# Optimization experiments

Measured on AMD Instinct MI355X. Metric: run time of the kernel, lower is better.

Reference implementation:

```python
import jax, jax.numpy as jnp
import numpy as np

ROT = 0.7071  # matches the literal used in DiagPool's affine theta
EPS = 1e-5    # GroupNorm default eps


def conv2d(x, w, pad):
    # x: (N,C,H,W), w: (O,I,kh,kw)
    return jax.lax.conv_general_dilated(
        x, w, window_strides=(1, 1), padding=[(pad, pad), (pad, pad)],
        dimension_numbers=("NCHW", "OIHW", "NCHW"))


def diag_pool(x):
    """Replicates F.affine_grid + F.grid_sample (align_corners=False, bilinear,
    zeros padding) with a 45-degree rotation, then mean over H (keepdim)."""
    N, C, H, W = x.shape
    dt = x.dtype
    xn = ((2.0 * jnp.arange(W, dtype=dt) + 1.0) / W - 1.0)  # normalized x coords
    yn = ((2.0 * jnp.arange(H, dtype=dt) + 1.0) / H - 1.0)  # normalized y coords
    Yn, Xn = jnp.meshgrid(yn, xn, indexing="ij")            # (H,W)
    xs = ROT * Xn - ROT * Yn   # theta row 0
    ys = ROT * Xn + ROT * Yn   # theta row 1
    # unnormalize (align_corners=False)
    xp = ((xs + 1.0) * W - 1.0) * 0.5
    yp = ((ys + 1.0) * H - 1.0) * 0.5
    x0 = jnp.floor(xp); y0 = jnp.floor(yp)
    x1 = x0 + 1.0;      y1 = y0 + 1.0
    wx1 = xp - x0; wx0 = 1.0 - wx1
    wy1 = yp - y0; wy0 = 1.0 - wy1

    def gather(yi, xi):
        valid = ((yi >= 0) & (yi < H) & (xi >= 0) & (xi < W)).astype(dt)
        yc = jnp.clip(yi, 0, H - 1).astype(jnp.int32)
        xc = jnp.clip(xi, 0, W - 1).astype(jnp.int32)
        return x[:, :, yc, xc] * valid  # (N,C,H,W)

    rot = (gather(y0, x0) * (wy0 * wx0) + gather(y0, x1) * (wy0 * wx1)
           + gather(y1, x0) * (wy1 * wx0) + gather(y1, x1) * (wy1 * wx1))
    return rot.mean(axis=2, keepdims=True)  # (N,C,1,W)


def group_norm_per_channel(x, g, b):
    # GroupNorm(cg, cg): each channel normalized over its own (H,W)
    mu = x.mean(axis=(2, 3), keepdims=True)
    var = x.var(axis=(2, 3), keepdims=True)
    xh = (x - mu) * jax.lax.rsqrt(var + EPS)
    return xh * g[None, :, None, None] + b[None, :, None, None]


def cross_axis_encode(gx, axis_fuse_w, gn_w, gn_b):
    N, cg, H, W = gx.shape
    x_h = gx.mean(axis=3, keepdims=True)                 # (N,cg,H,1)
    x_w = gx.mean(axis=2, keepdims=True)                 # (N,cg,1,W)
    x_d = diag_pool(gx)                                  # (N,cg,1,W)
    fused = jnp.concatenate(
        [x_h, x_w.transpose(0, 1, 3, 2), x_d.transpose(0, 1, 3, 2)], axis=2)  # (N,cg,H+2W,1)
    fused = conv2d(fused, axis_fuse_w, 0)
    x_h2 = fused[:, :, :H]          # (N,cg,H,1)
    x_w2 = fused[:, :, H:H + W]     # (N,cg,W,1)
    out = gx * jax.nn.sigmoid(x_h2) * jax.nn.sigmoid(x_w2.transpose(0, 1, 3, 2))
    return group_norm_per_channel(out, gn_w, gn_b)


def setup_inputs() -> dict:
    key = jax.random.key(0)
    B, C, H, W = 8, 256, 128, 128
    G = 32
    cg = C // G  # 8
    ks = jax.random.split(key, 10)
    s = 0.1
    return {
        "x": jax.random.normal(ks[0], (B, C, H, W), jnp.float32),
        "axis_fuse_w": jax.random.normal(ks[1], (cg, cg, 1, 1), jnp.float32) * s,
        "gn_w": jnp.ones((cg,), jnp.float32),
        "gn_b": jnp.zeros((cg,), jnp.float32),
        "conv1x1_w": jax.random.normal(ks[2], (cg, cg, 1, 1), jnp.float32) * s,
        "conv3x3_w": jax.random.normal(ks[3], (cg, cg, 3, 3), jnp.float32) * s,
        "conv5x5_w": jax.random.normal(ks[4], (cg, cg, 5, 5), jnp.float32) * s,
        "scale_w": jnp.ones((3,), jnp.float32),
        "ch_gate_w": jax.random.normal(ks[5], (cg, cg, 1, 1), jnp.float32) * s,
        "sp_gate_w": jax.random.normal(ks[6], (1, cg, 1, 1), jnp.float32) * s,
        "groups": 32,
    }


def reference(x, axis_fuse_w, gn_w, gn_b, conv1x1_w, conv3x3_w, conv5x5_w,
              scale_w, ch_gate_w, sp_gate_w, groups):
    B, C, H, W = x.shape
    cg = C // groups
    N = B * groups
    gx = x.reshape(N, cg, H, W)

    xa = cross_axis_encode(gx, axis_fuse_w, gn_w, gn_b)
    xa = conv2d(xa, conv1x1_w, 0)
    xb = conv2d(gx, conv3x3_w, 1)
    xc = conv2d(gx, conv5x5_w, 2)

    sw = jax.nn.softmax(scale_w)
    x1 = sw[0] * xa + sw[1] * xb + sw[2] * xc
    x2 = xb

    def ch_gate(t):
        return jax.nn.sigmoid(conv2d(t.mean(axis=(2, 3), keepdims=True), ch_gate_w, 0))

    def sp_gate(t):
        return jax.nn.sigmoid(conv2d(t, sp_gate_w, 0))

    x1 = x1 * ch_gate(x1) * sp_gate(x1)
    x2 = x2 * ch_gate(x2) * sp_gate(x2)

    x11 = jax.nn.softmax(x1.mean(axis=(2, 3)).reshape(N, 1, cg), axis=-1)  # (N,1,cg)
    x12 = x2.reshape(N, cg, H * W)
    x21 = jax.nn.softmax(x2.mean(axis=(2, 3)).reshape(N, 1, cg), axis=-1)
    x22 = x1.reshape(N, cg, H * W)
    weights = (x11 @ x12 + x21 @ x22).reshape(N, 1, H, W)
    return (gx * jax.nn.sigmoid(weights)).reshape(B, C, H, W)
```

## Files before the change

### kernel.cpp

```cpp
#include <hip/hip_runtime.h>
#include <math.h>

#define HH 128
#define WW 128
#define CG 8
#define NN 256
#define HWSZ (HH*WW)

typedef __bf16 bf16x8 __attribute__((ext_vector_type(8)));
typedef short short8v __attribute__((ext_vector_type(8)));
typedef float f32x4 __attribute__((ext_vector_type(4)));

__device__ __forceinline__ float sigmoidf_(float x){ return 1.0f/(1.0f+__expf(-x)); }

__device__ __forceinline__ unsigned short f2bf(float x){
  union { float f; unsigned u; } v; v.f = x;
  unsigned r = v.u + 0x7fffu + ((v.u >> 16) & 1u);
  return (unsigned short)(r >> 16);
}
__device__ __forceinline__ float bf2f(unsigned short h){
  union { unsigned u; float f; } v; v.u = ((unsigned)h) << 16; return v.f;
}

__global__ void kW(const float* __restrict__ w5, const float* __restrict__ scw,
                   float* __restrict__ w5s){
  int i = blockIdx.x*256 + threadIdx.x;
  if (i >= CG*CG*25) return;
  float a = scw[0], b = scw[1], c = scw[2];
  float m = fmaxf(a, fmaxf(b, c));
  float e0 = __expf(a-m), e1 = __expf(b-m), e2 = __expf(c-m);
  float sw2 = e2 / (e0+e1+e2);
  w5s[i] = sw2 * w5[i];
}

__global__ __launch_bounds__(256) void kA1(const float* __restrict__ gx,
                                           float* __restrict__ xh_ws,
                                           float* __restrict__ xw_ws){
  int b = blockIdx.x; int n = b >> 3; int c = b & 7;
  int tid = threadIdx.x;
  __shared__ float colpart[2][WW];
  const float* img = gx + (size_t)(n*CG+c)*HWSZ;
  int w = tid & 127, half = tid >> 7;
  float acc = 0.f;
  const float* p = img + half*64*WW + w;
  for (int h = 0; h < 64; ++h) acc += p[h*WW];
  colpart[half][w] = acc;
  int h2 = tid >> 1, wh = tid & 1;
  float racc = 0.f;
  const float* rp = img + h2*WW + wh*64;
  for (int j = 0; j < 64; ++j) racc += rp[j];
  racc += __shfl_xor(racc, 1);
  __syncthreads();
  if (tid < WW) xw_ws[(n*CG+c)*WW + tid] = (colpart[0][tid] + colpart[1][tid]) * (1.0f/HH);
  if (wh == 0) xh_ws[(n*CG+c)*HH + h2] = racc * (1.0f/WW);
}

__global__ __launch_bounds__(256) void kA2(const float* __restrict__ xh_ws,
                                           const float* __restrict__ xw_ws,
                                           const float* __restrict__ afw,
                                           float* __restrict__ sig_h,
                                           float* __restrict__ sig_w){
  int n = blockIdx.x;
  int tid = threadIdx.x;
  if (tid < HH){
    int h = tid;
    float v[CG];
    #pragma unroll
    for (int c = 0; c < CG; ++c) v[c] = xh_ws[(n*CG+c)*HH + h];
    #pragma unroll
    for (int o = 0; o < CG; ++o){
      float s = 0.f;
      #pragma unroll
      for (int i = 0; i < CG; ++i) s = fmaf(afw[o*CG+i], v[i], s);
      sig_h[(n*CG+o)*HH + h] = sigmoidf_(s);
    }
  } else {
    int w = tid - 128;
    float v[CG];
    #pragma unroll
    for (int c = 0; c < CG; ++c) v[c] = xw_ws[(n*CG+c)*WW + w];
    #pragma unroll
    for (int o = 0; o < CG; ++o){
      float s = 0.f;
      #pragma unroll
      for (int i = 0; i < CG; ++i) s = fmaf(afw[o*CG+i], v[i], s);
      sig_w[(n*CG+o)*WW + w] = sigmoidf_(s);
    }
  }
}

__global__ __launch_bounds__(256) void kB(const float* __restrict__ gx,
                                          const float* __restrict__ sig_h,
                                          const float* __restrict__ sig_w,
                                          const float* __restrict__ gn_w,
                                          const float* __restrict__ gn_b,
                                          float* __restrict__ Agn,
                                          float* __restrict__ Bgn){
  int b = blockIdx.x; int n = b >> 3; int c = b & 7;
  int tid = threadIdx.x;
  __shared__ float sh[HH];
  __shared__ float swv[WW];
  __shared__ float red[16];
  if (tid < HH) sh[tid] = sig_h[(n*CG+c)*HH + tid];
  else          swv[tid-128] = sig_w[(n*CG+c)*WW + tid - 128];
  __syncthreads();
  const float* img = gx + (size_t)(n*CG+c)*HWSZ;
  float s1 = 0.f, s2 = 0.f;
  for (int idx = tid; idx < HWSZ; idx += 256){
    int h = idx >> 7, w = idx & 127;
    float t = img[idx] * sh[h] * swv[w];
    s1 += t; s2 = fmaf(t, t, s2);
  }
  #pragma unroll
  for (int off = 32; off; off >>= 1){ s1 += __shfl_down(s1, off); s2 += __shfl_down(s2, off); }
  int wv = tid >> 6, ln = tid & 63;
  if (ln == 0){ red[wv] = s1; red[8+wv] = s2; }
  __syncthreads();
  if (tid == 0){
    float S1 = red[0]+red[1]+red[2]+red[3];
    float S2 = red[8]+red[9]+red[10]+red[11];
    float mu  = S1 * (1.0f/HWSZ);
    float var = S2 * (1.0f/HWSZ) - mu*mu;
    float rstd = rsqrtf(var + 1e-5f);
    float A = rstd * gn_w[c];
    Agn[n*CG+c] = A;
    Bgn[n*CG+c] = gn_b[c] - mu*A;
  }
}

__global__ __launch_bounds__(256) void kC(const float* __restrict__ gx,
                                          const float* __restrict__ w1,
                                          const float* __restrict__ w3,
                                          const float* __restrict__ w5s,
                                          const float* __restrict__ scale_w,
                                          const float* __restrict__ spw,
                                          const float* __restrict__ sig_h,
                                          const float* __restrict__ sig_w,
                                          const float* __restrict__ Agn,
                                          const float* __restrict__ Bgn,
                                          unsigned short* __restrict__ x1m,
                                          unsigned short* __restrict__ x2m,
                                          float* __restrict__ gacc){
  __shared__ __align__(16) unsigned short tile[68*36*8];
  __shared__ __align__(16) unsigned short Bm[7][16][32];
  __shared__ __align__(16) unsigned short BmLo[7][8][32];
  __shared__ float sighs[CG][32];
  __shared__ float sigws[CG][32];
  __shared__ float constA[CG];
  __shared__ float wred[4][32];

  int tid = threadIdx.x;
  int bb = blockIdx.x;
  int n  = bb >> 4;
  int t_ = bb & 15;
  int y0 = (t_ >> 2) * 32;
  int x0 = (t_ & 3) * 32;

  float sw0, sw1;
  {
    float a = scale_w[0], b = scale_w[1], c = scale_w[2];
    float m = fmaxf(a, fmaxf(b, c));
    float e0 = __expf(a-m), e1 = __expf(b-m), e2 = __expf(c-m);
    float inv = 1.0f/(e0+e1+e2);
    sw0 = e0*inv; sw1 = e1*inv;
  }
  {
    int ic = tid >> 5, k = tid & 31;
    sighs[ic][k] = sig_h[(n*CG+ic)*HH + y0 + k];
    sigws[ic][k] = sig_w[(n*CG+ic)*WW + x0 + k];
  }
  if (tid < CG){
    float s = 0.f;
    #pragma unroll
    for (int i = 0; i < CG; ++i) s = fmaf(w1[tid*CG+i], Bgn[n*CG+i], s);
    constA[tid] = sw0 * s;
  }

  const float* base_n = gx + (size_t)n*CG*HWSZ;
  #pragma unroll
  for (int p = 0; p < 4; ++p){
    const float* i0 = base_n + (size_t)(2*p)*HWSZ;
    const float* i1 = base_n + (size_t)(2*p+1)*HWSZ;
    for (int e = tid; e < 1296; e += 256){
      int yy = e / 36, xx = e - yy*36;
      int gy = y0 + yy - 2, gz = x0 + xx - 2;
      float v0 = 0.f, v1 = 0.f;
      if ((unsigned)gy < HH && (unsigned)gz < WW){
        int o = gy*WW + gz; v0 = i0[o]; v1 = i1[o];
      }
      unsigned pk = (unsigned)f2bf(v0) | ((unsigned)f2bf(v1) << 16);
      *reinterpret_cast<unsigned*>(&tile[(yy*36 + xx)*8 + 2*p]) = pk;
    }
  }

  for (int e = tid; e < 3584; e += 256){
    int s   = e >> 9;
    int rem = e & 511;
    int nn = rem >> 5, kk = rem & 31;
    int tap = s*4 + (kk >> 3);
    int ic  = kk & 7;
    float wv = 0.f;
    if (nn < 8){
      if (tap < 25)       wv = w5s[nn*200 + ic*25 + tap];
      else if (tap == 25) wv = sw0 * w1[nn*CG + ic] * Agn[n*CG + ic];
    } else if (tap < 25){
      int ky = tap/5, kx = tap - ky*5;
      if (ky >= 1 && ky <= 3 && kx >= 1 && kx <= 3)
        wv = w3[(nn-8)*72 + ic*9 + (ky-1)*3 + (kx-1)];
    }
    unsigned short hi = f2bf(wv);
    Bm[s][nn][kk] = hi;
    if (nn < 8) BmLo[s][nn][kk] = f2bf(wv - bf2f(hi));
  }
  __syncthreads();

  #pragma unroll
  for (int p = 0; p < 4; ++p){
    for (int e = tid; e < 1024; e += 256){
      int yl = e >> 5, xl = e & 31;
      unsigned pk = *reinterpret_cast<const unsigned*>(&tile[((yl+2)*36 + xl+2)*8 + 2*p]);
      float v0 = bf2f((unsigned short)(pk & 0xffffu)) * sighs[2*p][yl]   * sigws[2*p][xl];
      float v1 = bf2f((unsigned short)(pk >> 16))     * sighs[2*p+1][yl] * sigws[2*p+1][xl];
      unsigned opk = (unsigned)f2bf(v0) | ((unsigned)f2bf(v1) << 16);
      *reinterpret_cast<unsigned*>(&tile[((yl+36)*36 + xl+2)*8 + 2*p]) = opk;
    }
  }

  int lane = tid & 63;
  int wid  = tid >> 6;
  int pr = lane & 15;
  int tg = lane >> 4;
  short8v zs = {0,0,0,0,0,0,0,0};
  bf16x8 zb = __builtin_bit_cast(bf16x8, zs);
  bf16x8 bH[7], bL[7];
  int ofs[7];
  #pragma unroll
  for (int s = 0; s < 7; ++s){
    bH[s] = *reinterpret_cast<const bf16x8*>(&Bm[s][pr][tg*8]);
    bL[s] = (pr < 8) ? *reinterpret_cast<const bf16x8*>(&BmLo[s][pr][tg*8]) : zb;
    int t = s*4 + tg;
    int ky, kx;
    if (t < 25){ ky = t/5; kx = t - ky*5; }
    else if (t == 25){ ky = 36; kx = 2; }
    else { ky = 0; kx = 0; }
    ofs[s] = (ky*36 + kx)*8;
  }
  __syncthreads();

  float cA  = (pr < 8) ? constA[pr] : 0.f;
  float spv = spw[pr & 7];
  float sAcc = 0.f, qAcc = 0.f;

  #pragma unroll 2
  for (int i = 0; i < 16; ++i){
    int mb = wid*16 + i;
    int yl = mb >> 1;
    int xh = (mb & 1) << 4;
    const unsigned short* abase = &tile[(yl*36 + xh + pr)*8];
    f32x4 accP = {0.f,0.f,0.f,0.f};
    f32x4 accQ = {0.f,0.f,0.f,0.f};
    #pragma unroll
    for (int s = 0; s < 7; ++s){
      bf16x8 a = *reinterpret_cast<const bf16x8*>(abase + ofs[s]);
      accP = __builtin_amdgcn_mfma_f32_16x16x32_bf16(a, bH[s], accP, 0, 0, 0);
      accQ = __builtin_amdgcn_mfma_f32_16x16x32_bf16(a, bL[s], accQ, 0, 0, 0);
    }
    float av[4], ot[4], vv[4], sg[4];
    #pragma unroll
    for (int r = 0; r < 4; ++r) av[r] = accP[r] + accQ[r];
    #pragma unroll
    for (int r = 0; r < 4; ++r) ot[r] = __shfl_xor(av[r], 8);
    #pragma unroll
    for (int r = 0; r < 4; ++r)
      vv[r] = (pr < 8) ? (av[r] + cA + sw1*ot[r]) : av[r];
    #pragma unroll
    for (int r = 0; r < 4; ++r){
      float t = spv * vv[r];
      t += __shfl_xor(t, 1);
      t += __shfl_xor(t, 2);
      t += __shfl_xor(t, 4);
      sg[r] = sigmoidf_(t);
    }
    ushort4 u;
    #pragma unroll
    for (int r = 0; r < 4; ++r){
      sAcc += vv[r];
      qAcc = fmaf(vv[r], sg[r], qAcc);
      ((unsigned short*)&u)[r] = f2bf(vv[r]);
    }
    int gy  = y0 + yl;
    int gxx = x0 + xh + tg*4;
    size_t off = ((size_t)(n*CG + (pr & 7))*HH + gy)*WW + gxx;
    if (pr < 8) *reinterpret_cast<ushort4*>(x1m + off) = u;
    else        *reinterpret_cast<ushort4*>(x2m + off) = u;
  }

  sAcc += __shfl_xor(sAcc, 16); sAcc += __shfl_xor(sAcc, 32);
  qAcc += __shfl_xor(qAcc, 16); qAcc += __shfl_xor(qAcc, 32);
  if (lane < 16){
    int b0 = (pr < 8) ? pr : (8 + pr);
    wred[wid][b0]     = sAcc;
    wred[wid][b0 + 8] = qAcc;
  }
  __syncthreads();
  if (tid < 32){
    float s = wred[0][tid] + wred[1][tid] + wred[2][tid] + wred[3][tid];
    atomicAdd(&gacc[n*32 + tid], s);
  }
}

__global__ void kT(const float* __restrict__ gacc, const float* __restrict__ cgw,
                   float* __restrict__ a1a2){
  int n = blockIdx.x*blockDim.x + threadIdx.x;
  if (n >= NN) return;
  const float* g = gacc + n*32;
  float m1[CG], q1[CG], m2[CG], q2[CG];
  #pragma unroll
  for (int c = 0; c < CG; ++c){
    m1[c] = g[c]      * (1.0f/HWSZ);
    q1[c] = g[8+c]    * (1.0f/HWSZ);
    m2[c] = g[16+c]   * (1.0f/HWSZ);
    q2[c] = g[24+c]   * (1.0f/HWSZ);
  }
  float chg1[CG], chg2[CG];
  #pragma unroll
  for (int o = 0; o < CG; ++o){
    float s1 = 0.f, s2 = 0.f;
    #pragma unroll
    for (int i = 0; i < CG; ++i){ s1 = fmaf(cgw[o*CG+i], m1[i], s1); s2 = fmaf(cgw[o*CG+i], m2[i], s2); }
    chg1[o] = sigmoidf_(s1); chg2[o] = sigmoidf_(s2);
  }
  float z1[CG], z2[CG];
  float mx1 = -1e30f, mx2 = -1e30f;
  #pragma unroll
  for (int c = 0; c < CG; ++c){
    z1[c] = chg1[c]*q1[c]; z2[c] = chg2[c]*q2[c];
    mx1 = fmaxf(mx1, z1[c]); mx2 = fmaxf(mx2, z2[c]);
  }
  float su1 = 0.f, su2 = 0.f;
  #pragma unroll
  for (int c = 0; c < CG; ++c){
    z1[c] = __expf(z1[c]-mx1); su1 += z1[c];
    z2[c] = __expf(z2[c]-mx2); su2 += z2[c];
  }
  float i1 = 1.0f/su1, i2 = 1.0f/su2;
  #pragma unroll
  for (int c = 0; c < CG; ++c){
    float x11 = z1[c]*i1;
    float x21 = z2[c]*i2;
    a1a2[n*16 + c]     = x21 * chg1[c];
    a1a2[n*16 + 8 + c] = x11 * chg2[c];
  }
}

__global__ __launch_bounds__(256) void kF(const float* __restrict__ gx,
                                          const unsigned short* __restrict__ x1m,
                                          const unsigned short* __restrict__ x2m,
                                          const float* __restrict__ a1a2,
                                          const float* __restrict__ spw,
                                          float* __restrict__ out){
  int tid = threadIdx.x;
  int bb = blockIdx.x;
  int n  = bb >> 6;
  int hw = ((bb & 63) << 8) + tid;
  size_t base = (size_t)(n*CG)*HWSZ + hw;
  float a1[CG], a2[CG], sp[CG];
  #pragma unroll
  for (int c = 0; c < CG; ++c){
    a1[c] = a1a2[n*16 + c];
    a2[c] = a1a2[n*16 + 8 + c];
    sp[c] = spw[c];
  }
  float d1 = 0.f, dd1 = 0.f, d2 = 0.f, dd2 = 0.f;
  #pragma unroll
  for (int c = 0; c < CG; ++c){
    float v1 = bf2f(x1m[base + (size_t)c*HWSZ]);
    float v2 = bf2f(x2m[base + (size_t)c*HWSZ]);
    d1  = fmaf(sp[c], v1, d1);  dd1 = fmaf(a1[c], v1, dd1);
    d2  = fmaf(sp[c], v2, d2);  dd2 = fmaf(a2[c], v2, dd2);
  }
  float Wv = sigmoidf_(d1)*dd1 + sigmoidf_(d2)*dd2;
  float sW = sigmoidf_(Wv);
  #pragma unroll
  for (int c = 0; c < CG; ++c)
    out[base + (size_t)c*HWSZ] = gx[base + (size_t)c*HWSZ] * sW;
}

extern "C" void kernel_launch(void* const* d_in, const int* in_sizes, int n_in,
                              void* d_out, int out_size, void* d_ws, size_t ws_size,
                              hipStream_t stream){
  const float* x   = (const float*)d_in[0];
  const float* afw = (const float*)d_in[1];
  const float* gnw = (const float*)d_in[2];
  const float* gnb = (const float*)d_in[3];
  const float* w1  = (const float*)d_in[4];
  const float* w3  = (const float*)d_in[5];
  const float* w5  = (const float*)d_in[6];
  const float* scw = (const float*)d_in[7];
  const float* cgw = (const float*)d_in[8];
  const float* spw = (const float*)d_in[9];

  char* ws = (char*)d_ws;
  float* sig_h = (float*)(ws + 0);
  float* sig_w = (float*)(ws + 1048576);
  float* Agn   = (float*)(ws + 2097152);
  float* Bgn   = (float*)(ws + 2105344);
  float* gacc  = (float*)(ws + 2113536);
  float* a1a2  = (float*)(ws + 2146304);
  float* w5s   = (float*)(ws + 2146304);
  unsigned short* x1m = (unsigned short*)(ws + 2162688);
  unsigned short* x2m = (unsigned short*)(ws + 2162688 + 67108864);
  float* out = (float*)d_out;
  float* xh_ws = (float*)d_out;
  float* xw_ws = (float*)d_out + 262144;

  hipMemsetAsync(gacc, 0, NN*32*sizeof(float), stream);
  kW <<<7, 256, 0, stream>>>(w5, scw, w5s);
  kA1<<<NN*CG, 256, 0, stream>>>(x, xh_ws, xw_ws);
  kA2<<<NN, 256, 0, stream>>>(xh_ws, xw_ws, afw, sig_h, sig_w);
  kB <<<NN*CG, 256, 0, stream>>>(x, sig_h, sig_w, gnw, gnb, Agn, Bgn);
  kC <<<NN*16, 256, 0, stream>>>(x, w1, w3, w5s, scw, spw, sig_h, sig_w, Agn, Bgn, x1m, x2m, gacc);
  kT <<<4, 64, 0, stream>>>(gacc, cgw, a1a2);
  kF <<<NN*64, 256, 0, stream>>>(x, x1m, x2m, a1a2, spw, out);
}
```

Baseline: 506.8 us.

## Fold scale mixing and spatial-gate dot into MFMA weights; vectorize tile and final kernel

```diff
diff --git a/kernel.cpp b/kernel.cpp
--- a/kernel.cpp
+++ b/kernel.cpp
@@ -14,9 +14,8 @@
 __device__ __forceinline__ float sigmoidf_(float x){ return 1.0f/(1.0f+__expf(-x)); }
 
 __device__ __forceinline__ unsigned short f2bf(float x){
-  union { float f; unsigned u; } v; v.f = x;
-  unsigned r = v.u + 0x7fffu + ((v.u >> 16) & 1u);
-  return (unsigned short)(r >> 16);
+  __bf16 h = (__bf16)x;
+  return __builtin_bit_cast(unsigned short, h);
 }
 __device__ __forceinline__ float bf2f(unsigned short h){
   union { unsigned u; float f; } v; v.u = ((unsigned)h) << 16; return v.f;
@@ -143,7 +142,7 @@
                                           float* __restrict__ gacc){
   __shared__ __align__(16) unsigned short tile[68*36*8];
   __shared__ __align__(16) unsigned short Bm[7][16][32];
-  __shared__ __align__(16) unsigned short BmLo[7][8][32];
+  __shared__ __align__(16) unsigned short BmLo[7][10][32];
   __shared__ float sighs[CG][32];
   __shared__ float sigws[CG][32];
   __shared__ float constA[CG];
@@ -177,20 +176,23 @@
   }
 
   const float* base_n = gx + (size_t)n*CG*HWSZ;
-  #pragma unroll
-  for (int p = 0; p < 4; ++p){
-    const float* i0 = base_n + (size_t)(2*p)*HWSZ;
-    const float* i1 = base_n + (size_t)(2*p+1)*HWSZ;
-    for (int e = tid; e < 1296; e += 256){
-      int yy = e / 36, xx = e - yy*36;
-      int gy = y0 + yy - 2, gz = x0 + xx - 2;
-      float v0 = 0.f, v1 = 0.f;
-      if ((unsigned)gy < HH && (unsigned)gz < WW){
-        int o = gy*WW + gz; v0 = i0[o]; v1 = i1[o];
+  for (int e = tid; e < 1296; e += 256){
+    int yy = e / 36, xx = e - yy*36;
+    int gy = y0 + yy - 2, gz = x0 + xx - 2;
+    uint4 pk;
+    unsigned* pw = (unsigned*)&pk;
+    if ((unsigned)gy < HH && (unsigned)gz < WW){
+      int o = gy*WW + gz;
+      #pragma unroll
+      for (int p = 0; p < 4; ++p){
+        float v0 = base_n[(size_t)(2*p)*HWSZ + o];
+        float v1 = base_n[(size_t)(2*p+1)*HWSZ + o];
+        pw[p] = (unsigned)f2bf(v0) | ((unsigned)f2bf(v1) << 16);
       }
-      unsigned pk = (unsigned)f2bf(v0) | ((unsigned)f2bf(v1) << 16);
-      *reinterpret_cast<unsigned*>(&tile[(yy*36 + xx)*8 + 2*p]) = pk;
-    }
+    } else {
+      pw[0] = pw[1] = pw[2] = pw[3] = 0u;
+    }
+    *reinterpret_cast<uint4*>(&tile[e*8]) = pk;
   }
 
   for (int e = tid; e < 3584; e += 256){
@@ -199,31 +201,66 @@
     int nn = rem >> 5, kk = rem & 31;
     int tap = s*4 + (kk >> 3);
     int ic  = kk & 7;
+    int ky = tap/5, kx = tap - ky*5;
+    bool in3 = (tap < 25) && (ky >= 1) && (ky <= 3) && (kx >= 1) && (kx <= 3);
     float wv = 0.f;
     if (nn < 8){
-      if (tap < 25)       wv = w5s[nn*200 + ic*25 + tap];
-      else if (tap == 25) wv = sw0 * w1[nn*CG + ic] * Agn[n*CG + ic];
-    } else if (tap < 25){
-      int ky = tap/5, kx = tap - ky*5;
-      if (ky >= 1 && ky <= 3 && kx >= 1 && kx <= 3)
-        wv = w3[(nn-8)*72 + ic*9 + (ky-1)*3 + (kx-1)];
-    }
-    unsigned short hi = f2bf(wv);
-    Bm[s][nn][kk] = hi;
-    if (nn < 8) BmLo[s][nn][kk] = f2bf(wv - bf2f(hi));
-  }
-  __syncthreads();
-
-  #pragma unroll
-  for (int p = 0; p < 4; ++p){
-    for (int e = tid; e < 1024; e += 256){
-      int yl = e >> 5, xl = e & 31;
-      unsigned pk = *reinterpret_cast<const unsigned*>(&tile[((yl+2)*36 + xl+2)*8 + 2*p]);
-      float v0 = bf2f((unsigned short)(pk & 0xffffu)) * sighs[2*p][yl]   * sigws[2*p][xl];
-      float v1 = bf2f((unsigned short)(pk >> 16))     * sighs[2*p+1][yl] * sigws[2*p+1][xl];
-      unsigned opk = (unsigned)f2bf(v0) | ((unsigned)f2bf(v1) << 16);
-      *reinterpret_cast<unsigned*>(&tile[((yl+36)*36 + xl+2)*8 + 2*p]) = opk;
-    }
+      if (tap < 25){
+        wv = w5s[nn*200 + ic*25 + tap];
+        if (in3) wv = fmaf(sw1, w3[nn*72 + ic*9 + (ky-1)*3 + (kx-1)], wv);
+      } else if (tap == 25){
+        wv = sw0 * w1[nn*CG + ic] * Agn[n*CG + ic];
+      }
+      unsigned short hi = f2bf(wv);
+      Bm[s][nn][kk]   = hi;
+      BmLo[s][nn][kk] = f2bf(wv - bf2f(hi));
+    } else {
+      if (in3) wv = w3[(nn-8)*72 + ic*9 + (ky-1)*3 + (kx-1)];
+      Bm[s][nn][kk] = f2bf(wv);
+    }
+  }
+  for (int e = tid; e < 448; e += 256){
+    int s   = e >> 6;
+    int rem = e & 63;
+    int col = rem >> 5;
+    int kk  = rem & 31;
+    int tap = s*4 + (kk >> 3);
+    int ic  = kk & 7;
+    int ky = tap/5, kx = tap - ky*5;
+    bool in3 = (tap < 25) && (ky >= 1) && (ky <= 3) && (kx >= 1) && (kx <= 3);
+    float sum = 0.f;
+    #pragma unroll
+    for (int oc = 0; oc < 8; ++oc){
+      float wv = 0.f;
+      if (col == 0){
+        if (tap < 25){
+          wv = w5s[oc*200 + ic*25 + tap];
+          if (in3) wv = fmaf(sw1, w3[oc*72 + ic*9 + (ky-1)*3 + (kx-1)], wv);
+        } else if (tap == 25){
+          wv = sw0 * w1[oc*CG + ic] * Agn[n*CG + ic];
+        }
+      } else {
+        if (in3) wv = w3[oc*72 + ic*9 + (ky-1)*3 + (kx-1)];
+      }
+      sum = fmaf(spw[oc], wv, sum);
+    }
+    BmLo[s][8+col][kk] = f2bf(sum);
+  }
+  __syncthreads();
+
+  for (int e = tid; e < 1024; e += 256){
+    int yl = e >> 5, xl = e & 31;
+    uint4 pk = *reinterpret_cast<const uint4*>(&tile[((yl+2)*36 + (xl+2))*8]);
+    unsigned* pw = (unsigned*)&pk;
+    #pragma unroll
+    for (int p = 0; p < 4; ++p){
+      float g0 = sighs[2*p][yl]   * sigws[2*p][xl];
+      float g1 = sighs[2*p+1][yl] * sigws[2*p+1][xl];
+      float v0 = bf2f((unsigned short)(pw[p] & 0xffffu)) * g0;
+      float v1 = bf2f((unsigned short)(pw[p] >> 16))     * g1;
+      pw[p] = (unsigned)f2bf(v0) | ((unsigned)f2bf(v1) << 16);
+    }
+    *reinterpret_cast<uint4*>(&tile[((yl+36)*36 + (xl+2))*8]) = pk;
   }
 
   int lane = tid & 63;
@@ -237,7 +274,7 @@
   #pragma unroll
   for (int s = 0; s < 7; ++s){
     bH[s] = *reinterpret_cast<const bf16x8*>(&Bm[s][pr][tg*8]);
-    bL[s] = (pr < 8) ? *reinterpret_cast<const bf16x8*>(&BmLo[s][pr][tg*8]) : zb;
+    bL[s] = (pr < 10) ? *reinterpret_cast<const bf16x8*>(&BmLo[s][pr][tg*8]) : zb;
     int t = s*4 + tg;
     int ky, kx;
     if (t < 25){ ky = t/5; kx = t - ky*5; }
@@ -245,10 +282,13 @@
     else { ky = 0; kx = 0; }
     ofs[s] = (ky*36 + kx)*8;
   }
-  __syncthreads();
-
-  float cA  = (pr < 8) ? constA[pr] : 0.f;
-  float spv = spw[pr & 7];
+  float Cd1 = 0.f;
+  #pragma unroll
+  for (int oc = 0; oc < CG; ++oc) Cd1 = fmaf(spw[oc], constA[oc], Cd1);
+  __syncthreads();
+
+  float cA   = (pr < 8) ? constA[pr] : 0.f;
+  int  gsrc  = (lane & 48) | (pr < 8 ? 8 : 9);
   float sAcc = 0.f, qAcc = 0.f;
 
   #pragma unroll 2
@@ -265,28 +305,18 @@
       accP = __builtin_amdgcn_mfma_f32_16x16x32_bf16(a, bH[s], accP, 0, 0, 0);
       accQ = __builtin_amdgcn_mfma_f32_16x16x32_bf16(a, bL[s], accQ, 0, 0, 0);
     }
-    float av[4], ot[4], vv[4], sg[4];
-    #pragma unroll
-    for (int r = 0; r < 4; ++r) av[r] = accP[r] + accQ[r];
-    #pragma unroll
-    for (int r = 0; r < 4; ++r) ot[r] = __shfl_xor(av[r], 8);
-    #pragma unroll
-    for (int r = 0; r < 4; ++r)
-      vv[r] = (pr < 8) ? (av[r] + cA + sw1*ot[r]) : av[r];
+    float gq[4];
+    #pragma unroll
+    for (int r = 0; r < 4; ++r) gq[r] = __shfl(accQ[r], gsrc);
+    ushort4 u;
     #pragma unroll
     for (int r = 0; r < 4; ++r){
-      float t = spv * vv[r];
-      t += __shfl_xor(t, 1);
-      t += __shfl_xor(t, 2);
-      t += __shfl_xor(t, 4);
-      sg[r] = sigmoidf_(t);
-    }
-    ushort4 u;
-    #pragma unroll
-    for (int r = 0; r < 4; ++r){
-      sAcc += vv[r];
-      qAcc = fmaf(vv[r], sg[r], qAcc);
-      ((unsigned short*)&u)[r] = f2bf(vv[r]);
+      float vvr = (pr < 8) ? (accP[r] + accQ[r] + cA) : accP[r];
+      float d   = (pr < 8) ? (gq[r] + Cd1) : gq[r];
+      float sg  = sigmoidf_(d);
+      sAcc += vvr;
+      qAcc = fmaf(vvr, sg, qAcc);
+      ((unsigned short*)&u)[r] = f2bf(vvr);
     }
     int gy  = y0 + yl;
     int gxx = x0 + xh + tg*4;
@@ -361,8 +391,8 @@
                                           float* __restrict__ out){
   int tid = threadIdx.x;
   int bb = blockIdx.x;
-  int n  = bb >> 6;
-  int hw = ((bb & 63) << 8) + tid;
+  int n  = bb >> 4;
+  int hw = ((bb & 15) << 10) + tid*4;
   size_t base = (size_t)(n*CG)*HWSZ + hw;
   float a1[CG], a2[CG], sp[CG];
   #pragma unroll
@@ -371,19 +401,33 @@
     a2[c] = a1a2[n*16 + 8 + c];
     sp[c] = spw[c];
   }
-  float d1 = 0.f, dd1 = 0.f, d2 = 0.f, dd2 = 0.f;
-  #pragma unroll
-  for (int c = 0; c < CG; ++c){
-    float v1 = bf2f(x1m[base + (size_t)c*HWSZ]);
-    float v2 = bf2f(x2m[base + (size_t)c*HWSZ]);
-    d1  = fmaf(sp[c], v1, d1);  dd1 = fmaf(a1[c], v1, dd1);
-    d2  = fmaf(sp[c], v2, d2);  dd2 = fmaf(a2[c], v2, dd2);
-  }
-  float Wv = sigmoidf_(d1)*dd1 + sigmoidf_(d2)*dd2;
-  float sW = sigmoidf_(Wv);
-  #pragma unroll
-  for (int c = 0; c < CG; ++c)
-    out[base + (size_t)c*HWSZ] = gx[base + (size_t)c*HWSZ] * sW;
+  float d1[4]  = {0.f,0.f,0.f,0.f}, dd1[4] = {0.f,0.f,0.f,0.f};
+  float d2[4]  = {0.f,0.f,0.f,0.f}, dd2[4] = {0.f,0.f,0.f,0.f};
+  #pragma unroll
+  for (int c = 0; c < CG; ++c){
+    ushort4 u1 = *reinterpret_cast<const ushort4*>(x1m + base + (size_t)c*HWSZ);
+    ushort4 u2 = *reinterpret_cast<const ushort4*>(x2m + base + (size_t)c*HWSZ);
+    #pragma unroll
+    for (int p = 0; p < 4; ++p){
+      float v1 = bf2f(((const unsigned short*)&u1)[p]);
+      float v2 = bf2f(((const unsigned short*)&u2)[p]);
+      d1[p]  = fmaf(sp[c], v1, d1[p]);  dd1[p] = fmaf(a1[c], v1, dd1[p]);
+      d2[p]  = fmaf(sp[c], v2, d2[p]);  dd2[p] = fmaf(a2[c], v2, dd2[p]);
+    }
+  }
+  float sW[4];
+  #pragma unroll
+  for (int p = 0; p < 4; ++p){
+    float Wv = sigmoidf_(d1[p])*dd1[p] + sigmoidf_(d2[p])*dd2[p];
+    sW[p] = sigmoidf_(Wv);
+  }
+  #pragma unroll
+  for (int c = 0; c < CG; ++c){
+    float4 g = *reinterpret_cast<const float4*>(gx + base + (size_t)c*HWSZ);
+    float4 o;
+    o.x = g.x*sW[0]; o.y = g.y*sW[1]; o.z = g.z*sW[2]; o.w = g.w*sW[3];
+    *reinterpret_cast<float4*>(out + base + (size_t)c*HWSZ) = o;
+  }
 }
 
 extern "C" void kernel_launch(void* const* d_in, const int* in_sizes, int n_in,
@@ -421,5 +465,5 @@
   kB <<<NN*CG, 256, 0, stream>>>(x, sig_h, sig_w, gnw, gnb, Agn, Bgn);
   kC <<<NN*16, 256, 0, stream>>>(x, w1, w3, w5s, scw, spw, sig_h, sig_w, Agn, Bgn, x1m, x2m, gacc);
   kT <<<4, 64, 0, stream>>>(gacc, cgw, a1a2);
-  kF <<<NN*64, 256, 0, stream>>>(x, x1m, x2m, a1a2, spw, out);
-}
+  kF <<<NN*16, 256, 0, stream>>>(x, x1m, x2m, a1a2, spw, out);
+}
```

New measurement: 486.6 us. 4.0% less time.
